# Optimization experiments

Measured on AMD Instinct MI355X. Metric: run time of the kernel, lower is better.

Reference implementation:

```python
import jax, jax.numpy as jnp
import numpy as np
import math

N_HEADS = 16
EMBED = 1024
D_HEAD = EMBED // N_HEADS
B, L = 2, 2048


def setup_inputs() -> dict:
    key = jax.random.key(0)
    k1, k2, k3, k4, k5 = jax.random.split(key, 5)
    s = 0.02
    return {
        "x": jax.random.normal(k1, (B, L, EMBED), dtype=jnp.float32),
        "w_qkv": jax.random.normal(k2, (3 * EMBED, EMBED), dtype=jnp.float32) * s,
        "b_qkv": jax.random.normal(k3, (3 * EMBED,), dtype=jnp.float32) * s,
        "w_out": jax.random.normal(k4, (EMBED, EMBED), dtype=jnp.float32) * s,
        "b_out": jax.random.normal(k5, (EMBED,), dtype=jnp.float32) * s,
        "mask": 1,
    }


def reference(x, w_qkv, b_qkv, w_out, b_out, mask):
    b, l, e = x.shape
    qkv = x @ w_qkv.T + b_qkv                      # (B, L, 3E)
    q, k, v = jnp.split(qkv, 3, axis=-1)
    # (B, L, H, d) -> (B, H, L, d)
    q = q.reshape(b, l, N_HEADS, D_HEAD).transpose(0, 2, 1, 3)
    k = k.reshape(b, l, N_HEADS, D_HEAD).transpose(0, 2, 1, 3)
    v = v.reshape(b, l, N_HEADS, D_HEAD).transpose(0, 2, 1, 3)
    # NOTE: faithful to source bug -- scores use V, not K
    scores = jnp.einsum("bhld,bhmd->bhlm", q, v) * (1.0 / math.sqrt(D_HEAD))
    if mask:
        causal = jnp.triu(jnp.ones((l, l), dtype=bool), k=1)  # (L, L)
        scores = jnp.where(causal, -jnp.inf, scores)
    attn = jax.nn.softmax(scores, axis=-1)          # (B, H, L, L)
    out = jnp.einsum("bhlm,bhmd->bhld", attn, v)    # (B, H, L, d)
    # NOTE: faithful to source bug -- transpose(1,2) result discarded,
    # so reshape straight from (B, H, L, d) to (B, L, E)
    out = out.reshape(b, l, e)
    return out @ w_out.T + b_out
```

## Files before the change

### kernel.cpp

```cpp
#include <hip/hip_runtime.h>
#include <math.h>

constexpr int Lc = 2048, Ec = 1024, Hc = 16, Dc = 64;

typedef __attribute__((ext_vector_type(8))) short bf16x8;
typedef __attribute__((ext_vector_type(4))) float f32x4;
typedef unsigned short u16;
typedef unsigned int u32;

#define MFMA16(a, b, c) __builtin_amdgcn_mfma_f32_16x16x32_bf16(a, b, c, 0, 0, 0)

__device__ inline u16 f2bf(float f) {
  u32 u = __builtin_bit_cast(u32, f);
  u32 r = u + 0x7fff + ((u >> 16) & 1);
  return (u16)(r >> 16);
}

__device__ inline void gld16(const void* g, void* l) {
  __builtin_amdgcn_global_load_lds(
      (const __attribute__((address_space(1))) u32*)g,
      (__attribute__((address_space(3))) u32*)l, 16, 0, 0);
}

constexpr size_t XN = (size_t)4096 * 1024;
constexpr size_t WQN = (size_t)2048 * 1024;
constexpr size_t WON = (size_t)1024 * 1024;

__global__ __launch_bounds__(256) void convert_all(
    const float* __restrict__ x, const float* __restrict__ wqkv,
    const float* __restrict__ wout, u16* __restrict__ xb,
    u16* __restrict__ wqb, u16* __restrict__ wob)
{
  const size_t i = ((size_t)blockIdx.x * 256 + threadIdx.x) * 4;
  float4 v;
  u16* dst;
  if (i < XN) {
    v = *(const float4*)(x + i);
    dst = xb + i;
  } else if (i < XN + WQN) {
    const size_t off = i - XN;
    const size_t row = off >> 10, col = off & 1023;
    const size_t srow = row + ((row >> 10) << 10);
    v = *(const float4*)(wqkv + srow * 1024 + col);
    dst = wqb + off;
  } else {
    const size_t off = i - XN - WQN;
    v = *(const float4*)(wout + off);
    dst = wob + off;
  }
  u16 o0 = f2bf(v.x), o1 = f2bf(v.y), o2 = f2bf(v.z), o3 = f2bf(v.w);
  dst[0] = o0; dst[1] = o1; dst[2] = o2; dst[3] = o3;
}

__global__ __launch_bounds__(256) void gemm_qv(
    const u16* __restrict__ A, const u16* __restrict__ W,
    const float* __restrict__ bqkv, u16* __restrict__ Q, u16* __restrict__ V)
{
  __shared__ u16 As[128 * 32];
  __shared__ u16 Bs[128 * 32];
  const int tid = threadIdx.x;
  const int w = tid >> 6, lane = tid & 63;
  const int quad = lane >> 4, l16 = lane & 15;
  const int wm = w >> 1, wn = w & 1;
  const int rowTile = blockIdx.y * 128;
  const int colTile = blockIdx.x * 128;

  const int r0 = tid >> 2, o0 = (tid & 3) * 8;
  const u16* Ab0 = A + (size_t)(rowTile + r0) * 1024 + o0;
  const u16* Ab1 = A + (size_t)(rowTile + r0 + 64) * 1024 + o0;
  const u16* Bb0 = W + (size_t)(colTile + r0) * 1024 + o0;
  const u16* Bb1 = W + (size_t)(colTile + r0 + 64) * 1024 + o0;
  u16* lA0 = &As[(size_t)tid * 8];
  u16* lA1 = &As[(size_t)(tid + 256) * 8];
  u16* lB0 = &Bs[(size_t)tid * 8];
  u16* lB1 = &Bs[(size_t)(tid + 256) * 8];

  f32x4 acc[4][4] = {};

  for (int k0 = 0; k0 < 1024; k0 += 32) {
    __syncthreads();
    gld16(Ab0 + k0, lA0);
    gld16(Ab1 + k0, lA1);
    gld16(Bb0 + k0, lB0);
    gld16(Bb1 + k0, lB1);
    __syncthreads();
    bf16x8 af[4], bf[4];
#pragma unroll
    for (int s = 0; s < 4; ++s)
      af[s] = *(const bf16x8*)&As[(wm * 64 + s * 16 + l16) * 32 + quad * 8];
#pragma unroll
    for (int n = 0; n < 4; ++n)
      bf[n] = *(const bf16x8*)&Bs[(wn * 64 + n * 16 + l16) * 32 + quad * 8];
#pragma unroll
    for (int s = 0; s < 4; ++s)
#pragma unroll
      for (int n = 0; n < 4; ++n)
        acc[s][n] = MFMA16(af[s], bf[n], acc[s][n]);
  }

#pragma unroll
  for (int n = 0; n < 4; ++n) {
    const int gn = colTile + wn * 64 + n * 16 + l16;
    const bool isV = gn >= 1024;
    const float bias = bqkv[gn + (isV ? 1024 : 0)];
    const float scl = isV ? 1.0f : 0.125f;
    const int h = (gn & 1023) >> 6, d = gn & 63;
    u16* dst = isV ? V : Q;
#pragma unroll
    for (int s = 0; s < 4; ++s) {
#pragma unroll
      for (int r = 0; r < 4; ++r) {
        const int gm = rowTile + wm * 64 + s * 16 + quad * 4 + r;
        const int b = gm >> 11, l = gm & 2047;
        dst[(((size_t)(b * Hc + h)) * Lc + l) * Dc + d] = f2bf((acc[s][n][r] + bias) * scl);
      }
    }
  }
}

constexpr int VTSTR = 72;
constexpr int PSTR = 88;

__global__ __launch_bounds__(256, 1) void attn_mfma(
    const u16* __restrict__ Q, const u16* __restrict__ V,
    u16* __restrict__ outA)
{
  __shared__ u16 VsT[64 * VTSTR];
  __shared__ u16 Ps[256 * PSTR];
  const int tid = threadIdx.x;
  const int w = tid >> 6, lane = tid & 63;
  const int quad = lane >> 4, l16 = lane & 15;
  const int q0 = blockIdx.x * 256;
  const int bh = blockIdx.y;
  const int b = bh >> 4, h = bh & 15;
  const u16* Qb = Q + (size_t)bh * Lc * Dc;
  const u16* Vb = V + (size_t)bh * Lc * Dc;
  const int wq0 = q0 + w * 64;
  const int nt = (q0 >> 6) + 4;

  bf16x8 qf[4][2];
#pragma unroll
  for (int s = 0; s < 4; ++s)
#pragma unroll
    for (int kk = 0; kk < 2; ++kk)
      qf[s][kk] = *(const bf16x8*)(Qb + (size_t)(wq0 + s * 16 + l16) * 64 + kk * 32 + quad * 8);

  f32x4 O[4][4] = {};
  float lsum[4] = {0.f, 0.f, 0.f, 0.f};

  const int vr0 = tid >> 3, vd0 = (tid & 7) * 8;
  bf16x8 v0 = *(const bf16x8*)(Vb + (size_t)vr0 * 64 + vd0);
  bf16x8 v1 = *(const bf16x8*)(Vb + (size_t)(vr0 + 32) * 64 + vd0);
  bf16x8 av[4][2];
#pragma unroll
  for (int nb = 0; nb < 4; ++nb)
#pragma unroll
    for (int kk = 0; kk < 2; ++kk)
      av[nb][kk] = *(const bf16x8*)(Vb + (size_t)(nb * 16 + l16) * 64 + kk * 32 + quad * 8);

  for (int t = 0; t < nt; ++t) {
    const int kt = t * 64;
    __syncthreads();
#pragma unroll
    for (int j = 0; j < 8; ++j) {
      const int d = vd0 + j, sw = d & 0x38;
      VsT[d * VTSTR + (vr0 ^ sw)] = (u16)v0[j];
      VsT[d * VTSTR + ((vr0 + 32) ^ sw)] = (u16)v1[j];
    }
    if (t + 1 < nt) {
      v0 = *(const bf16x8*)(Vb + (size_t)(kt + 64 + vr0) * 64 + vd0);
      v1 = *(const bf16x8*)(Vb + (size_t)(kt + 96 + vr0) * 64 + vd0);
    }
    __syncthreads();
    if (kt > wq0) continue;

    const bool diag = (kt == wq0);
#pragma unroll
    for (int s = 0; s < 4; ++s) {
      f32x4 sf[4] = {};
#pragma unroll
      for (int nb = 0; nb < 4; ++nb) {
        sf[nb] = MFMA16(av[nb][0], qf[s][0], sf[nb]);
        sf[nb] = MFMA16(av[nb][1], qf[s][1], sf[nb]);
      }
#pragma unroll
      for (int nb = 0; nb < 4; ++nb) {
        float p[4];
#pragma unroll
        for (int r = 0; r < 4; ++r) {
          float pv = __expf(sf[nb][r]);
          if (diag && (nb * 16 + quad * 4 + r > s * 16 + l16)) pv = 0.f;
          p[r] = pv;
          lsum[s] += pv;
        }
        const u32 lo = (u32)f2bf(p[0]) | ((u32)f2bf(p[1]) << 16);
        const u32 hi = (u32)f2bf(p[2]) | ((u32)f2bf(p[3]) << 16);
        *(uint2*)&Ps[(size_t)(w * 64 + s * 16 + l16) * PSTR + nb * 16 + quad * 4] =
            make_uint2(lo, hi);
      }
    }
    if (kt + 64 <= wq0) {
#pragma unroll
      for (int nb = 0; nb < 4; ++nb)
#pragma unroll
        for (int kk = 0; kk < 2; ++kk)
          av[nb][kk] = *(const bf16x8*)(Vb + (size_t)(kt + 64 + nb * 16 + l16) * 64 + kk * 32 + quad * 8);
    }
    __asm__ volatile("s_waitcnt lgkmcnt(0)");

    bf16x8 vt[4][2], pb[4][2];
#pragma unroll
    for (int db = 0; db < 4; ++db) {
      const int d = db * 16 + l16, sw = d & 0x38;
      vt[db][0] = *(const bf16x8*)&VsT[d * VTSTR + ((quad * 8) ^ sw)];
      vt[db][1] = *(const bf16x8*)&VsT[d * VTSTR + ((32 + quad * 8) ^ sw)];
    }
#pragma unroll
    for (int s = 0; s < 4; ++s) {
      pb[s][0] = *(const bf16x8*)&Ps[(size_t)(w * 64 + s * 16 + l16) * PSTR + quad * 8];
      pb[s][1] = *(const bf16x8*)&Ps[(size_t)(w * 64 + s * 16 + l16) * PSTR + 32 + quad * 8];
    }
#pragma unroll
    for (int db = 0; db < 4; ++db)
#pragma unroll
      for (int s = 0; s < 4; ++s) {
        O[db][s] = MFMA16(vt[db][0], pb[s][0], O[db][s]);
        O[db][s] = MFMA16(vt[db][1], pb[s][1], O[db][s]);
      }
  }

#pragma unroll
  for (int s = 0; s < 4; ++s) {
    float l = lsum[s];
    l += __shfl_xor(l, 16);
    l += __shfl_xor(l, 32);
    const float inv = 1.f / l;
    const int row = h * 128 + (wq0 >> 4) + s;
    const size_t base = ((size_t)b * Lc + row) * Ec;
#pragma unroll
    for (int db = 0; db < 4; ++db) {
      const u32 lo = (u32)f2bf(O[db][s][0] * inv) | ((u32)f2bf(O[db][s][1] * inv) << 16);
      const u32 hi = (u32)f2bf(O[db][s][2] * inv) | ((u32)f2bf(O[db][s][3] * inv) << 16);
      *(uint2*)(outA + base + l16 * 64 + db * 16 + quad * 4) = make_uint2(lo, hi);
    }
  }
}

__global__ __launch_bounds__(256) void gemm_out(
    const u16* __restrict__ A, const u16* __restrict__ W,
    const float* __restrict__ bias, float* __restrict__ out)
{
  __shared__ u16 As[64 * 32];
  __shared__ u16 Bs[128 * 32];
  const int tid = threadIdx.x;
  const int w = tid >> 6, lane = tid & 63;
  const int quad = lane >> 4, l16 = lane & 15;
  const int wm = w & 1, wn = w >> 1;
  const int rowTile = blockIdx.y * 64;
  const int colTile = blockIdx.x * 128;

  const int r0 = tid >> 2, o0 = (tid & 3) * 8;
  const u16* Ab0 = A + (size_t)(rowTile + r0) * 1024 + o0;
  const u16* Bb0 = W + (size_t)(colTile + r0) * 1024 + o0;
  const u16* Bb1 = W + (size_t)(colTile + r0 + 64) * 1024 + o0;
  u16* lA0 = &As[(size_t)tid * 8];
  u16* lB0 = &Bs[(size_t)tid * 8];
  u16* lB1 = &Bs[(size_t)(tid + 256) * 8];

  f32x4 acc[2][4] = {};

  for (int k0 = 0; k0 < 1024; k0 += 32) {
    __syncthreads();
    gld16(Ab0 + k0, lA0);
    gld16(Bb0 + k0, lB0);
    gld16(Bb1 + k0, lB1);
    __syncthreads();
    bf16x8 af[2], bf[4];
#pragma unroll
    for (int s = 0; s < 2; ++s)
      af[s] = *(const bf16x8*)&As[(wm * 32 + s * 16 + l16) * 32 + quad * 8];
#pragma unroll
    for (int n = 0; n < 4; ++n)
      bf[n] = *(const bf16x8*)&Bs[(wn * 64 + n * 16 + l16) * 32 + quad * 8];
#pragma unroll
    for (int s = 0; s < 2; ++s)
#pragma unroll
      for (int n = 0; n < 4; ++n)
        acc[s][n] = MFMA16(af[s], bf[n], acc[s][n]);
  }

#pragma unroll
  for (int n = 0; n < 4; ++n) {
    const int gn = colTile + wn * 64 + n * 16 + l16;
    const float bn = bias[gn];
#pragma unroll
    for (int s = 0; s < 2; ++s)
#pragma unroll
      for (int r = 0; r < 4; ++r) {
        const int gm = rowTile + wm * 32 + s * 16 + quad * 4 + r;
        out[(size_t)gm * 1024 + gn] = acc[s][n][r] + bn;
      }
  }
}

extern "C" void kernel_launch(void* const* d_in, const int* in_sizes, int n_in,
                              void* d_out, int out_size, void* d_ws, size_t ws_size,
                              hipStream_t stream) {
  (void)in_sizes; (void)n_in; (void)out_size; (void)ws_size;
  const float* x     = (const float*)d_in[0];
  const float* w_qkv = (const float*)d_in[1];
  const float* b_qkv = (const float*)d_in[2];
  const float* w_out = (const float*)d_in[3];
  const float* b_out = (const float*)d_in[4];
  float* out = (float*)d_out;

  u16* xb  = (u16*)d_ws;
  u16* wqb = xb + XN;
  u16* wob = wqb + WQN;
  u16* Qw  = wob + WON;
  u16* Vw  = Qw + (size_t)2 * Hc * Lc * Dc;
  u16* Aw  = Vw + (size_t)2 * Hc * Lc * Dc;

  convert_all<<<7168, 256, 0, stream>>>(x, w_qkv, w_out, xb, wqb, wob);
  gemm_qv<<<dim3(16, 32), 256, 0, stream>>>(xb, wqb, b_qkv, Qw, Vw);
  attn_mfma<<<dim3(8, 32), 256, 0, stream>>>(Qw, Vw, Aw);
  gemm_out<<<dim3(8, 64), 256, 0, stream>>>(Aw, wob, b_out, out);
}
```

Baseline: 209.8 us.

## Keep P in registers via k16 MFMA, pre-transpose V in QV GEMM

The QV projection GEMM now also writes a transposed copy of V, so the attention kernel can stage V^T into shared memory with plain vector stores instead of a scalar transposing swizzle. The attention kernel drops the shared-memory P buffer and feeds probabilities straight from the score accumulators into 16x16x16 bf16 MFMAs, whose operand layout matches the accumulator layout. Query tiles shrink to 128 rows with two blocks per CU, and are launched in reverse order so the longest causal tiles start first for better load balance. In exchange the projection does extra strided, uncoalesced writes for V^T and the workspace needs another buffer.

```diff
diff --git a/kernel.cpp b/kernel.cpp
--- a/kernel.cpp
+++ b/kernel.cpp
@@ -4,11 +4,21 @@
 constexpr int Lc = 2048, Ec = 1024, Hc = 16, Dc = 64;
 
 typedef __attribute__((ext_vector_type(8))) short bf16x8;
+typedef __attribute__((ext_vector_type(4))) short bf16x4;
 typedef __attribute__((ext_vector_type(4))) float f32x4;
 typedef unsigned short u16;
 typedef unsigned int u32;
 
-#define MFMA16(a, b, c) __builtin_amdgcn_mfma_f32_16x16x32_bf16(a, b, c, 0, 0, 0)
+#define MFMA32(a, b, c) __builtin_amdgcn_mfma_f32_16x16x32_bf16(a, b, c, 0, 0, 0)
+
+__device__ inline f32x4 mfma_k16(bf16x4 a, bf16x4 b, f32x4 c) {
+#if __has_builtin(__builtin_amdgcn_mfma_f32_16x16x16bf16_1k)
+  return __builtin_amdgcn_mfma_f32_16x16x16bf16_1k(a, b, c, 0, 0, 0);
+#else
+  asm("v_mfma_f32_16x16x16_bf16 %0, %1, %2, %0" : "+v"(c) : "v"(a), "v"(b));
+  return c;
+#endif
+}
 
 __device__ inline u16 f2bf(float f) {
   u32 u = __builtin_bit_cast(u32, f);
@@ -54,7 +64,8 @@
 
 __global__ __launch_bounds__(256) void gemm_qv(
     const u16* __restrict__ A, const u16* __restrict__ W,
-    const float* __restrict__ bqkv, u16* __restrict__ Q, u16* __restrict__ V)
+    const float* __restrict__ bqkv, u16* __restrict__ Q, u16* __restrict__ V,
+    u16* __restrict__ VT)
 {
   __shared__ u16 As[128 * 32];
   __shared__ u16 Bs[128 * 32];
@@ -95,13 +106,13 @@
     for (int s = 0; s < 4; ++s)
 #pragma unroll
       for (int n = 0; n < 4; ++n)
-        acc[s][n] = MFMA16(af[s], bf[n], acc[s][n]);
-  }
-
+        acc[s][n] = MFMA32(af[s], bf[n], acc[s][n]);
+  }
+
+  const bool isV = (colTile >= 1024);
 #pragma unroll
   for (int n = 0; n < 4; ++n) {
     const int gn = colTile + wn * 64 + n * 16 + l16;
-    const bool isV = gn >= 1024;
     const float bias = bqkv[gn + (isV ? 1024 : 0)];
     const float scl = isV ? 1.0f : 0.125f;
     const int h = (gn & 1023) >> 6, d = gn & 63;
@@ -112,45 +123,48 @@
       for (int r = 0; r < 4; ++r) {
         const int gm = rowTile + wm * 64 + s * 16 + quad * 4 + r;
         const int b = gm >> 11, l = gm & 2047;
-        dst[(((size_t)(b * Hc + h)) * Lc + l) * Dc + d] = f2bf((acc[s][n][r] + bias) * scl);
+        const u16 val = f2bf((acc[s][n][r] + bias) * scl);
+        const size_t bhh = (size_t)(b * Hc + h);
+        dst[(bhh * Lc + l) * Dc + d] = val;
+        if (isV) VT[(bhh * Dc + d) * Lc + l] = val;
       }
     }
   }
 }
 
-constexpr int VTSTR = 72;
-constexpr int PSTR = 88;
-
-__global__ __launch_bounds__(256, 1) void attn_mfma(
+constexpr int VTSTR = 68;
+
+__global__ __launch_bounds__(256, 2) void attn_mfma(
     const u16* __restrict__ Q, const u16* __restrict__ V,
-    u16* __restrict__ outA)
+    const u16* __restrict__ VT, u16* __restrict__ outA)
 {
   __shared__ u16 VsT[64 * VTSTR];
-  __shared__ u16 Ps[256 * PSTR];
   const int tid = threadIdx.x;
   const int w = tid >> 6, lane = tid & 63;
   const int quad = lane >> 4, l16 = lane & 15;
-  const int q0 = blockIdx.x * 256;
+  const int qt = 15 - (int)blockIdx.x;
+  const int q0 = qt * 128;
   const int bh = blockIdx.y;
   const int b = bh >> 4, h = bh & 15;
   const u16* Qb = Q + (size_t)bh * Lc * Dc;
   const u16* Vb = V + (size_t)bh * Lc * Dc;
-  const int wq0 = q0 + w * 64;
-  const int nt = (q0 >> 6) + 4;
-
-  bf16x8 qf[4][2];
-#pragma unroll
-  for (int s = 0; s < 4; ++s)
+  const u16* VTb = VT + (size_t)bh * Dc * Lc;
+  const int wq0 = q0 + w * 32;
+  const int nt = 2 * qt + 2;
+
+  bf16x8 qf[2][2];
+#pragma unroll
+  for (int s = 0; s < 2; ++s)
 #pragma unroll
     for (int kk = 0; kk < 2; ++kk)
       qf[s][kk] = *(const bf16x8*)(Qb + (size_t)(wq0 + s * 16 + l16) * 64 + kk * 32 + quad * 8);
 
-  f32x4 O[4][4] = {};
-  float lsum[4] = {0.f, 0.f, 0.f, 0.f};
-
-  const int vr0 = tid >> 3, vd0 = (tid & 7) * 8;
-  bf16x8 v0 = *(const bf16x8*)(Vb + (size_t)vr0 * 64 + vd0);
-  bf16x8 v1 = *(const bf16x8*)(Vb + (size_t)(vr0 + 32) * 64 + vd0);
+  f32x4 O[4][2] = {};
+  float lsum[2] = {0.f, 0.f};
+
+  const int sd = tid >> 2, sk = (tid & 3) * 16;
+  bf16x8 stg0 = *(const bf16x8*)(VTb + (size_t)sd * Lc + sk);
+  bf16x8 stg1 = *(const bf16x8*)(VTb + (size_t)sd * Lc + sk + 8);
   bf16x8 av[4][2];
 #pragma unroll
   for (int nb = 0; nb < 4; ++nb)
@@ -161,87 +175,77 @@
   for (int t = 0; t < nt; ++t) {
     const int kt = t * 64;
     __syncthreads();
-#pragma unroll
-    for (int j = 0; j < 8; ++j) {
-      const int d = vd0 + j, sw = d & 0x38;
-      VsT[d * VTSTR + (vr0 ^ sw)] = (u16)v0[j];
-      VsT[d * VTSTR + ((vr0 + 32) ^ sw)] = (u16)v1[j];
-    }
+    *(bf16x8*)&VsT[sd * VTSTR + sk] = stg0;
+    *(bf16x8*)&VsT[sd * VTSTR + sk + 8] = stg1;
     if (t + 1 < nt) {
-      v0 = *(const bf16x8*)(Vb + (size_t)(kt + 64 + vr0) * 64 + vd0);
-      v1 = *(const bf16x8*)(Vb + (size_t)(kt + 96 + vr0) * 64 + vd0);
-    }
-    __syncthreads();
-    if (kt > wq0) continue;
-
-    const bool diag = (kt == wq0);
-#pragma unroll
-    for (int s = 0; s < 4; ++s) {
-      f32x4 sf[4] = {};
+      stg0 = *(const bf16x8*)(VTb + (size_t)sd * Lc + kt + 64 + sk);
+      stg1 = *(const bf16x8*)(VTb + (size_t)sd * Lc + kt + 64 + sk + 8);
+    }
+    __syncthreads();
+    if (kt > wq0 + 31) continue;
+
+    f32x4 sf[2][4] = {};
+#pragma unroll
+    for (int s = 0; s < 2; ++s)
 #pragma unroll
       for (int nb = 0; nb < 4; ++nb) {
-        sf[nb] = MFMA16(av[nb][0], qf[s][0], sf[nb]);
-        sf[nb] = MFMA16(av[nb][1], qf[s][1], sf[nb]);
+        sf[s][nb] = MFMA32(av[nb][0], qf[s][0], sf[s][nb]);
+        sf[s][nb] = MFMA32(av[nb][1], qf[s][1], sf[s][nb]);
       }
+    if (kt + 64 <= wq0 + 31) {
+#pragma unroll
+      for (int nb = 0; nb < 4; ++nb)
+#pragma unroll
+        for (int kk = 0; kk < 2; ++kk)
+          av[nb][kk] = *(const bf16x8*)(Vb + (size_t)(kt + 64 + nb * 16 + l16) * 64 + kk * 32 + quad * 8);
+    }
+
+    bf16x4 vt[4][4];
+#pragma unroll
+    for (int nb = 0; nb < 4; ++nb)
+#pragma unroll
+      for (int db = 0; db < 4; ++db)
+        vt[nb][db] = *(const bf16x4*)&VsT[(db * 16 + l16) * VTSTR + nb * 16 + quad * 4];
+
+    const bool needmask = (kt + 63 > wq0);
+#pragma unroll
+    for (int s = 0; s < 2; ++s) {
+      bf16x4 pp[4];
 #pragma unroll
       for (int nb = 0; nb < 4; ++nb) {
         float p[4];
 #pragma unroll
         for (int r = 0; r < 4; ++r) {
-          float pv = __expf(sf[nb][r]);
-          if (diag && (nb * 16 + quad * 4 + r > s * 16 + l16)) pv = 0.f;
+          float pv = __expf(sf[s][nb][r]);
+          if (needmask && (kt + nb * 16 + quad * 4 + r > wq0 + s * 16 + l16)) pv = 0.f;
           p[r] = pv;
           lsum[s] += pv;
         }
-        const u32 lo = (u32)f2bf(p[0]) | ((u32)f2bf(p[1]) << 16);
-        const u32 hi = (u32)f2bf(p[2]) | ((u32)f2bf(p[3]) << 16);
-        *(uint2*)&Ps[(size_t)(w * 64 + s * 16 + l16) * PSTR + nb * 16 + quad * 4] =
-            make_uint2(lo, hi);
+        pp[nb] = (bf16x4){(short)f2bf(p[0]), (short)f2bf(p[1]),
+                          (short)f2bf(p[2]), (short)f2bf(p[3])};
       }
-    }
-    if (kt + 64 <= wq0) {
 #pragma unroll
       for (int nb = 0; nb < 4; ++nb)
 #pragma unroll
-        for (int kk = 0; kk < 2; ++kk)
-          av[nb][kk] = *(const bf16x8*)(Vb + (size_t)(kt + 64 + nb * 16 + l16) * 64 + kk * 32 + quad * 8);
-    }
-    __asm__ volatile("s_waitcnt lgkmcnt(0)");
-
-    bf16x8 vt[4][2], pb[4][2];
-#pragma unroll
-    for (int db = 0; db < 4; ++db) {
-      const int d = db * 16 + l16, sw = d & 0x38;
-      vt[db][0] = *(const bf16x8*)&VsT[d * VTSTR + ((quad * 8) ^ sw)];
-      vt[db][1] = *(const bf16x8*)&VsT[d * VTSTR + ((32 + quad * 8) ^ sw)];
-    }
-#pragma unroll
-    for (int s = 0; s < 4; ++s) {
-      pb[s][0] = *(const bf16x8*)&Ps[(size_t)(w * 64 + s * 16 + l16) * PSTR + quad * 8];
-      pb[s][1] = *(const bf16x8*)&Ps[(size_t)(w * 64 + s * 16 + l16) * PSTR + 32 + quad * 8];
-    }
-#pragma unroll
-    for (int db = 0; db < 4; ++db)
-#pragma unroll
-      for (int s = 0; s < 4; ++s) {
-        O[db][s] = MFMA16(vt[db][0], pb[s][0], O[db][s]);
-        O[db][s] = MFMA16(vt[db][1], pb[s][1], O[db][s]);
-      }
-  }
-
-#pragma unroll
-  for (int s = 0; s < 4; ++s) {
+        for (int db = 0; db < 4; ++db)
+          O[db][s] = mfma_k16(vt[nb][db], pp[nb], O[db][s]);
+    }
+  }
+
+#pragma unroll
+  for (int s = 0; s < 2; ++s) {
     float l = lsum[s];
     l += __shfl_xor(l, 16);
     l += __shfl_xor(l, 32);
     const float inv = 1.f / l;
-    const int row = h * 128 + (wq0 >> 4) + s;
-    const size_t base = ((size_t)b * Lc + row) * Ec;
+    const int q = wq0 + s * 16 + l16;
+    const int row = h * 128 + (q >> 4);
+    const size_t base = ((size_t)b * Lc + row) * Ec + ((q & 15) << 6);
 #pragma unroll
     for (int db = 0; db < 4; ++db) {
       const u32 lo = (u32)f2bf(O[db][s][0] * inv) | ((u32)f2bf(O[db][s][1] * inv) << 16);
       const u32 hi = (u32)f2bf(O[db][s][2] * inv) | ((u32)f2bf(O[db][s][3] * inv) << 16);
-      *(uint2*)(outA + base + l16 * 64 + db * 16 + quad * 4) = make_uint2(lo, hi);
+      *(uint2*)(outA + base + db * 16 + quad * 4) = make_uint2(lo, hi);
     }
   }
 }
@@ -286,7 +290,7 @@
     for (int s = 0; s < 2; ++s)
 #pragma unroll
       for (int n = 0; n < 4; ++n)
-        acc[s][n] = MFMA16(af[s], bf[n], acc[s][n]);
+        acc[s][n] = MFMA32(af[s], bf[n], acc[s][n]);
   }
 
 #pragma unroll
@@ -314,15 +318,17 @@
   const float* b_out = (const float*)d_in[4];
   float* out = (float*)d_out;
 
+  constexpr size_t QVN = (size_t)2 * Hc * Lc * Dc;
   u16* xb  = (u16*)d_ws;
   u16* wqb = xb + XN;
   u16* wob = wqb + WQN;
   u16* Qw  = wob + WON;
-  u16* Vw  = Qw + (size_t)2 * Hc * Lc * Dc;
-  u16* Aw  = Vw + (size_t)2 * Hc * Lc * Dc;
+  u16* Vw  = Qw + QVN;
+  u16* VTw = Vw + QVN;
+  u16* Aw  = VTw + QVN;
 
   convert_all<<<7168, 256, 0, stream>>>(x, w_qkv, w_out, xb, wqb, wob);
-  gemm_qv<<<dim3(16, 32), 256, 0, stream>>>(xb, wqb, b_qkv, Qw, Vw);
-  attn_mfma<<<dim3(8, 32), 256, 0, stream>>>(Qw, Vw, Aw);
+  gemm_qv<<<dim3(16, 32), 256, 0, stream>>>(xb, wqb, b_qkv, Qw, Vw, VTw);
+  attn_mfma<<<dim3(16, 32), 256, 0, stream>>>(Qw, Vw, VTw, Aw);
   gemm_out<<<dim3(8, 64), 256, 0, stream>>>(Aw, wob, b_out, out);
 }
```

New measurement: 209.3 us. About the same (-0.3%).
